# Kernel tuning notes

Measured on AMD Instinct MI355X. Metric: run time of the kernel, lower is better.

Reference implementation:

```python
import jax, jax.numpy as jnp
import numpy as np

N = 50000
IN_DIM = 512
OUT_DIM = 128
E = 800000
EPS = 1e-5


def setup_inputs() -> dict:
    key = jax.random.key(0)
    ks = jax.random.split(key, 12)
    x = jax.random.normal(ks[0], (N, IN_DIM), dtype=jnp.float32)
    edge_index = jax.random.randint(ks[1], (2, E), 0, N, dtype=jnp.int64)
    s1 = 1.0 / np.sqrt(IN_DIM)
    s2 = 1.0 / np.sqrt(OUT_DIM)
    W1 = jax.random.normal(ks[2], (IN_DIM, OUT_DIM), dtype=jnp.float32) * s1
    b1 = jnp.zeros((OUT_DIM,), jnp.float32)
    W2 = jax.random.normal(ks[3], (OUT_DIM, OUT_DIM), dtype=jnp.float32) * s2
    b2 = jnp.zeros((OUT_DIM,), jnp.float32)
    W3 = jax.random.normal(ks[4], (OUT_DIM, OUT_DIM), dtype=jnp.float32) * s2
    b3 = jnp.zeros((OUT_DIM,), jnp.float32)
    g1 = jnp.ones((OUT_DIM,), jnp.float32)
    be1 = jnp.zeros((OUT_DIM,), jnp.float32)
    g2 = jnp.ones((OUT_DIM,), jnp.float32)
    be2 = jnp.zeros((OUT_DIM,), jnp.float32)
    a1 = jnp.full((1,), 0.25, jnp.float32)  # PReLU weight
    a2 = jnp.full((1,), 0.25, jnp.float32)
    return {"x": x, "edge_index": edge_index, "W1": W1, "b1": b1, "W2": W2,
            "b2": b2, "W3": W3, "b3": b3, "g1": g1, "be1": be1, "g2": g2,
            "be2": be2, "a1": a1, "a2": a2}


def _gcn_norm(edge_index, n):
    # add self-loops, symmetric normalization deg^-1/2 A deg^-1/2
    loop = jnp.arange(n, dtype=edge_index.dtype)
    src = jnp.concatenate([edge_index[0], loop])
    dst = jnp.concatenate([edge_index[1], loop])
    deg = jax.ops.segment_sum(jnp.ones_like(dst, jnp.float32), dst, num_segments=n)
    dinv = jax.lax.rsqrt(jnp.maximum(deg, 1.0))
    norm = dinv[src] * dinv[dst]
    return src, dst, norm


def _gcn_conv(x, W, b, src, dst, norm, n):
    h = x @ W                                   # [N, out]
    msg = h[src] * norm[:, None]                # gather + scale over edges
    agg = jax.ops.segment_sum(msg, dst, num_segments=n)
    return agg + b


def _bn(x, g, b):
    mean = jnp.mean(x, axis=0)
    var = jnp.var(x, axis=0)  # biased, as torch BN uses for normalization
    return (x - mean) * jax.lax.rsqrt(var + EPS) * g + b


def _prelu(x, a):
    return jnp.where(x >= 0, x, a * x)


def reference(x, edge_index, W1, b1, W2, b2, W3, b3, g1, be1, g2, be2, a1, a2):
    src, dst, norm = _gcn_norm(edge_index, N)
    h = _gcn_conv(x, W1, b1, src, dst, norm, N)
    h = _prelu(_bn(h, g1, be1), a1)
    h = _gcn_conv(h, W2, b2, src, dst, norm, N)
    h = _prelu(_bn(h, g2, be2), a2)
    h = _gcn_conv(h, W3, b3, src, dst, norm, N)
    return h
```

## Files before the change

kernel.cpp:

```cpp
#include <hip/hip_runtime.h>

#define N_NODES 50000
#define IN_DIM  512
#define OUT_DIM 128
#define BN_EPS  1e-5f

typedef __attribute__((ext_vector_type(8))) short short8;
typedef __attribute__((ext_vector_type(4))) float f32x4;

__device__ __forceinline__ unsigned short bf16_rne(float x) {
    unsigned u = __float_as_uint(x);
    unsigned r = (u + 0x7FFFu + ((u >> 16) & 1u)) >> 16;
    return (unsigned short)r;
}
__device__ __forceinline__ float bf16_to_f(unsigned short s) {
    return __uint_as_float(((unsigned)s) << 16);
}

__device__ __forceinline__ void gload16(const void* g, void* l) {
    __builtin_amdgcn_global_load_lds(
        (const __attribute__((address_space(1))) void*)g,
        (__attribute__((address_space(3))) void*)l, 16, 0, 0);
}


__global__ void init_kernel(int* __restrict__ cnt, float* __restrict__ stats, int n) {
    int i = blockIdx.x * blockDim.x + threadIdx.x;
    if (i < n) cnt[i] = 1;
    if (i < 4096) stats[i] = 0.f;
}

__device__ __forceinline__ int edge_is64(const int* ei) {
    return (ei[1] | ei[3] | ei[5] | ei[7]) == 0;
}

__global__ void deg_kernel(const int* __restrict__ ei, int* __restrict__ cnt, int E) {
    int e = blockIdx.x * blockDim.x + threadIdx.x;
    if (e >= E) return;
    int dst;
    if (edge_is64(ei)) dst = ((const int2*)ei)[E + e].x;
    else               dst = ei[E + e];
    atomicAdd(&cnt[dst], 1);
}


__global__ __launch_bounds__(1024) void scan_partial(const int* __restrict__ cnt,
                                                     int* __restrict__ psum, int n) {
    __shared__ int wsum[16];
    const int i = blockIdx.x * 1024 + threadIdx.x;
    const int lane = threadIdx.x & 63;
    const int wv = threadIdx.x >> 6;
    int v = (i < n) ? cnt[i] : 0;
#pragma unroll
    for (int d = 1; d < 64; d <<= 1) v += __shfl_xor(v, d);
    if (lane == 0) wsum[wv] = v;
    __syncthreads();
    if (threadIdx.x == 0) {
        int t = 0;
#pragma unroll
        for (int w = 0; w < 16; ++w) t += wsum[w];
        psum[blockIdx.x] = t;
    }
}

__global__ void scan_base(const int* __restrict__ psum, int* __restrict__ pbase,
                          int* __restrict__ rowp, int nb, int n) {
    const int lane = threadIdx.x;
    int orig = (lane < nb) ? psum[lane] : 0;
    int v = orig;
#pragma unroll
    for (int d = 1; d < 64; d <<= 1) {
        int t = __shfl_up(v, d);
        if (lane >= d) v += t;
    }
    if (lane < nb) pbase[lane] = v - orig;
    if (lane == nb - 1) rowp[n] = v;
}

__global__ __launch_bounds__(1024) void scan_final(int* __restrict__ cnt,
                                                   const int* __restrict__ pbase,
                                                   int* __restrict__ rowp,
                                                   float* __restrict__ dinv,
                                                   unsigned short* __restrict__ col, int n) {
    __shared__ int wsum[16];
    const int i = blockIdx.x * 1024 + threadIdx.x;
    const int lane = threadIdx.x & 63;
    const int wv = threadIdx.x >> 6;
    int orig = (i < n) ? cnt[i] : 0;
    int v = orig;
#pragma unroll
    for (int d = 1; d < 64; d <<= 1) {
        int t = __shfl_up(v, d);
        if (lane >= d) v += t;
    }
    if (lane == 63) wsum[wv] = v;
    __syncthreads();
    int woff = 0;
    for (int w = 0; w < wv; ++w) woff += wsum[w];
    if (i < n) {
        int rp = pbase[blockIdx.x] + woff + v - orig;
        rowp[i] = rp;
        dinv[i] = rsqrtf(fmaxf((float)orig, 1.f));
        col[rp] = (unsigned short)i;
        cnt[i] = rp + 1;
    }
}

__global__ void fill_kernel(const int* __restrict__ ei, int* __restrict__ cnt,
                            unsigned short* __restrict__ col, int E) {
    int e = blockIdx.x * blockDim.x + threadIdx.x;
    if (e >= E) return;
    int src, dst;
    if (edge_is64(ei)) { src = ((const int2*)ei)[e].x; dst = ((const int2*)ei)[E + e].x; }
    else               { src = ei[e];                  dst = ei[E + e]; }
    int pos = atomicAdd(&cnt[dst], 1);
    col[pos] = (unsigned short)src;
}


__global__ __launch_bounds__(256) void wconv_all(const float* __restrict__ W1, short* __restrict__ Wt1,
                                                 const float* __restrict__ W2, short* __restrict__ Wt2,
                                                 const float* __restrict__ W3, short* __restrict__ Wt3) {
    __shared__ short tile[64][130];
    const int b = blockIdx.x;
    const float* W; short* Wt; int K, k0;
    if (b < 8)       { W = W1; Wt = Wt1; K = IN_DIM;  k0 = b * 64; }
    else if (b < 10) { W = W2; Wt = Wt2; K = OUT_DIM; k0 = (b - 8) * 64; }
    else             { W = W3; Wt = Wt3; K = OUT_DIM; k0 = (b - 10) * 64; }
    for (int i = threadIdx.x; i < 64 * 128; i += 256) {
        int k = i >> 7, c = i & 127;
        tile[k][c] = (short)bf16_rne(W[(size_t)(k0 + k) * 128 + c]);
    }
    __syncthreads();
    for (int i = threadIdx.x; i < 64 * 128; i += 256) {
        int c = i >> 6, k = i & 63;
        Wt[(size_t)c * K + k0 + k] = tile[k][c];
    }
}


template <typename TA, int K, bool XFORM>
__global__ __launch_bounds__(256) void mfma_gemm(
        const TA* __restrict__ A, const short* __restrict__ Wt,
        unsigned short* __restrict__ out, int M,
        const float* __restrict__ stats, const float* __restrict__ gam,
        const float* __restrict__ bet, const float* __restrict__ alpha_p,
        const float* __restrict__ dinv) {
    constexpr int BK = 64;
    constexpr int NSTEP = K / BK;
    constexpr int UPRA = (BK * (int)sizeof(TA)) / 16;
    constexpr int AINST = 64 * UPRA / 256;
    __shared__ TA    ldsA[64 * BK];
    __shared__ short ldsB[128 * BK];
    __shared__ float bnp[256];

    const int tid  = threadIdx.x;
    const int lane = tid & 63;
    const int wv   = tid >> 6;
    const int r16  = lane & 15;
    const int g    = lane >> 4;
    const int row0 = blockIdx.x * 64;
    const int arow_t = wv * 16 + r16;

    float alpha = 0.f;
    if constexpr (XFORM) {
        alpha = alpha_p[0];
        if (tid < 128) {
            float sum = 0.f, sq = 0.f;
#pragma unroll
            for (int r = 0; r < 8; ++r) {
                sum += stats[r * 256 + tid];
                sq  += stats[r * 256 + 128 + tid];
            }
            const float inv_n = 1.0f / (float)N_NODES;
            float mean = sum * inv_n;
            float var = fmaxf(sq * inv_n - mean * mean, 0.f);
            float sc = gam[tid] * rsqrtf(var + BN_EPS);
            bnp[tid] = sc;
            bnp[128 + tid] = bet[tid] - mean * sc;
        }
        __syncthreads();
    }

    f32x4 acc[8];
#pragma unroll
    for (int nf = 0; nf < 8; nf++) acc[nf] = (f32x4)(0.f);

    for (int s = 0; s < NSTEP; ++s) {
        const int k0 = s * BK;
        if (s) __syncthreads();
#pragma unroll
        for (int i = 0; i < AINST; ++i) {
            const int d   = i * 256 + tid;
            const int row = d / UPRA, p = d % UPRA;
            int grow = row0 + row; if (grow >= M) grow = M - 1;
            const char* src = (const char*)(A + (size_t)grow * K + k0) + ((p ^ (row & 7)) * 16);
            gload16(src, (char*)ldsA + (size_t)(i * 256 + wv * 64) * 16);
        }
#pragma unroll
        for (int i = 0; i < 4; ++i) {
            const int d    = i * 256 + tid;
            const int colb = d >> 3, p = d & 7;
            const short* src = Wt + (size_t)colb * K + k0 + (p ^ (colb & 7)) * 8;
            gload16(src, (char*)ldsB + (size_t)(i * 256 + wv * 64) * 16);
        }
        __syncthreads();
#pragma unroll
        for (int ksub = 0; ksub < 2; ++ksub) {
            short8 af;
            if constexpr (sizeof(TA) == 4) {
                const int q0 = ksub * 8 + g * 2;
                const float4* A4 = (const float4*)ldsA;
                float4 alo = A4[arow_t * UPRA + (q0 ^ (r16 & 7))];
                float4 ahi = A4[arow_t * UPRA + ((q0 + 1) ^ (r16 & 7))];
                float av[8] = {alo.x, alo.y, alo.z, alo.w, ahi.x, ahi.y, ahi.z, ahi.w};
#pragma unroll
                for (int j = 0; j < 8; j++) af[j] = (short)bf16_rne(av[j]);
            } else {
                short8 raw = ((const short8*)ldsA)[arow_t * 8 + ((ksub * 4 + g) ^ (r16 & 7))];
                if constexpr (XFORM) {
                    const int kk = ksub * 32 + g * 8;
                    const int kb = k0 + kk;
#pragma unroll
                    for (int j = 0; j < 8; j++) {
                        float v = fmaf(bf16_to_f((unsigned short)raw[j]), bnp[kb + j], bnp[128 + kb + j]);
                        v = v >= 0.f ? v : alpha * v;
                        af[j] = (short)bf16_rne(v);
                    }
                } else {
                    af = raw;
                }
            }
#pragma unroll
            for (int nf = 0; nf < 8; nf++) {
                const int colb = nf * 16 + r16;
                short8 bf = ((const short8*)ldsB)[colb * 8 + ((ksub * 4 + g) ^ (r16 & 7))];
                acc[nf] = __builtin_amdgcn_mfma_f32_16x16x32_bf16(af, bf, acc[nf], 0, 0, 0);
            }
        }
    }

    __syncthreads();
    unsigned short* ot = (unsigned short*)ldsB;
#pragma unroll
    for (int r = 0; r < 4; ++r) {
        const int trow = wv * 16 + g * 4 + r;
        const int grow = row0 + trow;
        const float dv = (grow < M) ? dinv[grow] : 0.f;
#pragma unroll
        for (int nf = 0; nf < 8; nf++)
            ot[trow * 128 + nf * 16 + r16] = bf16_rne(acc[nf][r] * dv);
    }
    __syncthreads();
    {
        const int trow = wv * 16 + r16;
        const int seg  = g;
        const int grow = row0 + trow;
        if (grow < M) {
            const float4* lsrc = (const float4*)ot + trow * 16 + seg * 4;
            float4* gdst = (float4*)((char*)out + (size_t)grow * 256) + seg * 4;
#pragma unroll
            for (int i = 0; i < 4; ++i) gdst[i] = lsrc[i];
        }
    }
}


template <int FINAL>
__global__ __launch_bounds__(256) void agg_kernel(
        const unsigned short* __restrict__ h, const int* __restrict__ rowp,
        const unsigned short* __restrict__ col, const float* __restrict__ dinv,
        const float* __restrict__ bias, void* __restrict__ outv,
        float* __restrict__ stats, int n) {
    const int wave = threadIdx.x >> 6;
    const int lane = threadIdx.x & 63;
    const int f = lane << 1;
    const float b0 = bias[f], b1 = bias[f + 1];
    float s0 = 0.f, s1 = 0.f, q0 = 0.f, q1 = 0.f;
    const int stride = gridDim.x << 2;
    for (int node = (blockIdx.x << 2) + wave; node < n; node += stride) {
        int e = rowp[node];
        const int end = rowp[node + 1];
        float a0 = 0.f, a1 = 0.f;
        for (; e + 8 <= end; e += 8) {
            int c[8];
#pragma unroll
            for (int j = 0; j < 8; j++) c[j] = col[e + j];
            unsigned v[8];
#pragma unroll
            for (int j = 0; j < 8; j++) v[j] = *(const unsigned*)(h + (size_t)c[j] * OUT_DIM + f);
#pragma unroll
            for (int j = 0; j < 8; j++) {
                a0 += __uint_as_float(v[j] << 16);
                a1 += __uint_as_float(v[j] & 0xFFFF0000u);
            }
        }
        for (; e < end; ++e) {
            unsigned v = *(const unsigned*)(h + (size_t)col[e] * OUT_DIM + f);
            a0 += __uint_as_float(v << 16);
            a1 += __uint_as_float(v & 0xFFFF0000u);
        }
        float dn = dinv[node];
        a0 = fmaf(a0, dn, b0);
        a1 = fmaf(a1, dn, b1);
        if (FINAL) {
            ((float2*)outv)[(size_t)node * 64 + lane] = make_float2(a0, a1);
        } else {
            unsigned p = ((unsigned)bf16_rne(a1) << 16) | (unsigned)bf16_rne(a0);
            ((unsigned*)outv)[(size_t)node * 64 + lane] = p;
            s0 += a0; s1 += a1;
            q0 = fmaf(a0, a0, q0); q1 = fmaf(a1, a1, q1);
        }
    }
    if (!FINAL) {
        __shared__ float red[4][256];
        red[wave][f] = s0;        red[wave][f + 1] = s1;
        red[wave][128 + f] = q0;  red[wave][128 + f + 1] = q1;
        __syncthreads();
        int t = threadIdx.x;
        float v = red[0][t] + red[1][t] + red[2][t] + red[3][t];
        atomicAdd(&stats[(blockIdx.x & 7) * 256 + t], v);
    }
}


extern "C" void kernel_launch(void* const* d_in, const int* in_sizes, int n_in,
                              void* d_out, int out_size, void* d_ws, size_t ws_size,
                              hipStream_t stream) {
    const float* x   = (const float*)d_in[0];
    const int*   ei  = (const int*)d_in[1];
    const float* W1  = (const float*)d_in[2];
    const float* b1  = (const float*)d_in[3];
    const float* W2  = (const float*)d_in[4];
    const float* b2  = (const float*)d_in[5];
    const float* W3  = (const float*)d_in[6];
    const float* b3  = (const float*)d_in[7];
    const float* g1  = (const float*)d_in[8];
    const float* be1 = (const float*)d_in[9];
    const float* g2  = (const float*)d_in[10];
    const float* be2 = (const float*)d_in[11];
    const float* a1  = (const float*)d_in[12];
    const float* a2  = (const float*)d_in[13];

    const int n = N_NODES;
    const int E = in_sizes[1] / 2;
    float* out = (float*)d_out;

    char* ws = (char*)d_ws;
    size_t off = 0;
    auto alloc = [&](size_t bytes) { void* p = ws + off; off += (bytes + 255) & ~(size_t)255; return p; };
    unsigned short* bufA = (unsigned short*)alloc((size_t)n * OUT_DIM * sizeof(short));
    unsigned short* hb   = (unsigned short*)alloc((size_t)n * OUT_DIM * sizeof(short));
    int*   cnt   = (int*)alloc((size_t)n * sizeof(int));
    int*   rowp  = (int*)alloc((size_t)(n + 1) * sizeof(int));
    float* dinv  = (float*)alloc((size_t)n * sizeof(float));
    unsigned short* col = (unsigned short*)alloc((size_t)(E + n) * sizeof(unsigned short));
    float* stats = (float*)alloc(4096 * sizeof(float));
    short* Wt1   = (short*)alloc((size_t)IN_DIM * OUT_DIM * sizeof(short));
    short* Wt2   = (short*)alloc((size_t)OUT_DIM * OUT_DIM * sizeof(short));
    short* Wt3   = (short*)alloc((size_t)OUT_DIM * OUT_DIM * sizeof(short));
    int*   psum  = (int*)alloc(64 * sizeof(int));
    int*   pbase = (int*)alloc(64 * sizeof(int));

    const int nbScan = (n + 1023) / 1024;

    hipLaunchKernelGGL(init_kernel, dim3((n + 255) / 256), dim3(256), 0, stream, cnt, stats, n);
    hipLaunchKernelGGL(deg_kernel, dim3((E + 255) / 256), dim3(256), 0, stream, ei, cnt, E);
    hipLaunchKernelGGL(scan_partial, dim3(nbScan), dim3(1024), 0, stream, cnt, psum, n);
    hipLaunchKernelGGL(scan_base, dim3(1), dim3(64), 0, stream, psum, pbase, rowp, nbScan, n);
    hipLaunchKernelGGL(scan_final, dim3(nbScan), dim3(1024), 0, stream, cnt, pbase, rowp, dinv, col, n);
    hipLaunchKernelGGL(fill_kernel, dim3((E + 255) / 256), dim3(256), 0, stream, ei, cnt, col, E);
    hipLaunchKernelGGL(wconv_all, dim3(12), dim3(256), 0, stream, W1, Wt1, W2, Wt2, W3, Wt3);

    const int gblocks = (n + 63) / 64;
    const int ablocks = 2048;
    hipLaunchKernelGGL((mfma_gemm<float, IN_DIM, false>), dim3(gblocks), dim3(256), 0, stream,
                       x, Wt1, bufA, n, nullptr, nullptr, nullptr, nullptr, dinv);
    hipLaunchKernelGGL((agg_kernel<0>), dim3(ablocks), dim3(256), 0, stream,
                       bufA, rowp, col, dinv, b1, hb, stats, n);
    hipLaunchKernelGGL((mfma_gemm<short, OUT_DIM, true>), dim3(gblocks), dim3(256), 0, stream,
                       (const short*)hb, Wt2, bufA, n, stats, g1, be1, a1, dinv);
    hipLaunchKernelGGL((agg_kernel<0>), dim3(ablocks), dim3(256), 0, stream,
                       bufA, rowp, col, dinv, b2, hb, stats + 2048, n);
    hipLaunchKernelGGL((mfma_gemm<short, OUT_DIM, true>), dim3(gblocks), dim3(256), 0, stream,
                       (const short*)hb, Wt3, bufA, n, stats + 2048, g2, be2, a2, dinv);
    hipLaunchKernelGGL((agg_kernel<1>), dim3(ablocks), dim3(256), 0, stream,
                       bufA, rowp, col, dinv, b3, out, nullptr, n);
}
```

Baseline: 280.9 us.

## Double-buffer GEMM LDS tiles and merge scan into single chained-lookback kernel

Replaces the three-kernel prefix scan (partial sums, base scan, final) with one kernel. Each block waits on its predecessor's inclusive sum through atomic acquire/release flags, which removes two launches. The GEMM now double-buffers its A and B LDS tiles so the next K-step's global-to-LDS loads are issued before the current step's MFMAs, overlapping memory with compute. The costs are twice the LDS (fp32 A for layer 1 becomes large), which may cut occupancy, and a serial spin chain in the scan that relies on blocks being scheduled in order.

```diff
diff --git a/kernel.cpp b/kernel.cpp
--- a/kernel.cpp
+++ b/kernel.cpp
@@ -1,4 +1,5 @@
 #include <hip/hip_runtime.h>
+#include <limits.h>
 
 #define N_NODES 50000
 #define IN_DIM  512
@@ -24,10 +25,12 @@
 }
 
 
-__global__ void init_kernel(int* __restrict__ cnt, float* __restrict__ stats, int n) {
+__global__ void init_kernel(int* __restrict__ cnt, float* __restrict__ stats,
+                            int* __restrict__ incl, int n) {
     int i = blockIdx.x * blockDim.x + threadIdx.x;
     if (i < n) cnt[i] = 1;
     if (i < 4096) stats[i] = 0.f;
+    if (i < 64) incl[i] = INT_MIN;
 }
 
 __device__ __forceinline__ int edge_is64(const int* ei) {
@@ -44,65 +47,47 @@
 }
 
 
-__global__ __launch_bounds__(1024) void scan_partial(const int* __restrict__ cnt,
-                                                     int* __restrict__ psum, int n) {
+__global__ __launch_bounds__(1024) void scan_lookback(int* __restrict__ cnt,
+                                                      int* __restrict__ incl,
+                                                      int* __restrict__ rowp,
+                                                      float* __restrict__ dinv,
+                                                      unsigned short* __restrict__ col, int n) {
     __shared__ int wsum[16];
-    const int i = blockIdx.x * 1024 + threadIdx.x;
-    const int lane = threadIdx.x & 63;
-    const int wv = threadIdx.x >> 6;
-    int v = (i < n) ? cnt[i] : 0;
-#pragma unroll
-    for (int d = 1; d < 64; d <<= 1) v += __shfl_xor(v, d);
-    if (lane == 0) wsum[wv] = v;
-    __syncthreads();
-    if (threadIdx.x == 0) {
-        int t = 0;
-#pragma unroll
-        for (int w = 0; w < 16; ++w) t += wsum[w];
-        psum[blockIdx.x] = t;
-    }
-}
-
-__global__ void scan_base(const int* __restrict__ psum, int* __restrict__ pbase,
-                          int* __restrict__ rowp, int nb, int n) {
-    const int lane = threadIdx.x;
-    int orig = (lane < nb) ? psum[lane] : 0;
+    __shared__ int sbase;
+    const int b = blockIdx.x;
+    const int tid = threadIdx.x;
+    const int i = b * 1024 + tid;
+    const int lane = tid & 63;
+    const int wv = tid >> 6;
+    int orig = (i < n) ? cnt[i] : 0;
     int v = orig;
 #pragma unroll
     for (int d = 1; d < 64; d <<= 1) {
         int t = __shfl_up(v, d);
         if (lane >= d) v += t;
     }
-    if (lane < nb) pbase[lane] = v - orig;
-    if (lane == nb - 1) rowp[n] = v;
-}
-
-__global__ __launch_bounds__(1024) void scan_final(int* __restrict__ cnt,
-                                                   const int* __restrict__ pbase,
-                                                   int* __restrict__ rowp,
-                                                   float* __restrict__ dinv,
-                                                   unsigned short* __restrict__ col, int n) {
-    __shared__ int wsum[16];
-    const int i = blockIdx.x * 1024 + threadIdx.x;
-    const int lane = threadIdx.x & 63;
-    const int wv = threadIdx.x >> 6;
-    int orig = (i < n) ? cnt[i] : 0;
-    int v = orig;
-#pragma unroll
-    for (int d = 1; d < 64; d <<= 1) {
-        int t = __shfl_up(v, d);
-        if (lane >= d) v += t;
-    }
     if (lane == 63) wsum[wv] = v;
     __syncthreads();
     int woff = 0;
     for (int w = 0; w < wv; ++w) woff += wsum[w];
+    if (tid == 1023) {
+        int base = 0;
+        if (b > 0) {
+            while ((base = __hip_atomic_load(&incl[b - 1], __ATOMIC_ACQUIRE,
+                                             __HIP_MEMORY_SCOPE_AGENT)) == INT_MIN) {}
+        }
+        __hip_atomic_store(&incl[b], base + woff + v, __ATOMIC_RELEASE,
+                           __HIP_MEMORY_SCOPE_AGENT);
+        sbase = base;
+    }
+    __syncthreads();
     if (i < n) {
-        int rp = pbase[blockIdx.x] + woff + v - orig;
+        int rp = sbase + woff + v - orig;
         rowp[i] = rp;
         dinv[i] = rsqrtf(fmaxf((float)orig, 1.f));
         col[rp] = (unsigned short)i;
         cnt[i] = rp + 1;
+        if (i == n - 1) rowp[n] = sbase + woff + v;
     }
 }
 
@@ -150,8 +135,8 @@
     constexpr int NSTEP = K / BK;
     constexpr int UPRA = (BK * (int)sizeof(TA)) / 16;
     constexpr int AINST = 64 * UPRA / 256;
-    __shared__ TA    ldsA[64 * BK];
-    __shared__ short ldsB[128 * BK];
+    __shared__ TA    ldsA[2][64 * BK];
+    __shared__ short ldsB[2][128 * BK];
     __shared__ float bnp[256];
 
     const int tid  = threadIdx.x;
@@ -161,6 +146,28 @@
     const int g    = lane >> 4;
     const int row0 = blockIdx.x * 64;
     const int arow_t = wv * 16 + r16;
+
+    auto stageA = [&](int bi, int k0) {
+#pragma unroll
+        for (int i = 0; i < AINST; ++i) {
+            const int d   = i * 256 + tid;
+            const int row = d / UPRA, p = d % UPRA;
+            int grow = row0 + row; if (grow >= M) grow = M - 1;
+            const char* src = (const char*)(A + (size_t)grow * K + k0) + ((p ^ (row & 7)) * 16);
+            gload16(src, (char*)ldsA[bi] + (size_t)(i * 256 + wv * 64) * 16);
+        }
+    };
+    auto stageB = [&](int bi, int k0) {
+#pragma unroll
+        for (int i = 0; i < 4; ++i) {
+            const int d    = i * 256 + tid;
+            const int colb = d >> 3, p = d & 7;
+            const short* src = Wt + (size_t)colb * K + k0 + (p ^ (colb & 7)) * 8;
+            gload16(src, (char*)ldsB[bi] + (size_t)(i * 256 + wv * 64) * 16);
+        }
+    };
+
+    stageA(0, 0); stageB(0, 0);
 
     float alpha = 0.f;
     if constexpr (XFORM) {
@@ -179,48 +186,36 @@
             bnp[tid] = sc;
             bnp[128 + tid] = bet[tid] - mean * sc;
         }
-        __syncthreads();
     }
 
     f32x4 acc[8];
 #pragma unroll
     for (int nf = 0; nf < 8; nf++) acc[nf] = (f32x4)(0.f);
 
+    __syncthreads();
+
     for (int s = 0; s < NSTEP; ++s) {
+        const int cur = s & 1;
+        if (s + 1 < NSTEP) {
+            stageA(cur ^ 1, (s + 1) * BK);
+            stageB(cur ^ 1, (s + 1) * BK);
+        }
         const int k0 = s * BK;
-        if (s) __syncthreads();
-#pragma unroll
-        for (int i = 0; i < AINST; ++i) {
-            const int d   = i * 256 + tid;
-            const int row = d / UPRA, p = d % UPRA;
-            int grow = row0 + row; if (grow >= M) grow = M - 1;
-            const char* src = (const char*)(A + (size_t)grow * K + k0) + ((p ^ (row & 7)) * 16);
-            gload16(src, (char*)ldsA + (size_t)(i * 256 + wv * 64) * 16);
-        }
-#pragma unroll
-        for (int i = 0; i < 4; ++i) {
-            const int d    = i * 256 + tid;
-            const int colb = d >> 3, p = d & 7;
-            const short* src = Wt + (size_t)colb * K + k0 + (p ^ (colb & 7)) * 8;
-            gload16(src, (char*)ldsB + (size_t)(i * 256 + wv * 64) * 16);
-        }
-        __syncthreads();
 #pragma unroll
         for (int ksub = 0; ksub < 2; ++ksub) {
             short8 af;
             if constexpr (sizeof(TA) == 4) {
                 const int q0 = ksub * 8 + g * 2;
-                const float4* A4 = (const float4*)ldsA;
+                const float4* A4 = (const float4*)ldsA[cur];
                 float4 alo = A4[arow_t * UPRA + (q0 ^ (r16 & 7))];
                 float4 ahi = A4[arow_t * UPRA + ((q0 + 1) ^ (r16 & 7))];
                 float av[8] = {alo.x, alo.y, alo.z, alo.w, ahi.x, ahi.y, ahi.z, ahi.w};
 #pragma unroll
                 for (int j = 0; j < 8; j++) af[j] = (short)bf16_rne(av[j]);
             } else {
-                short8 raw = ((const short8*)ldsA)[arow_t * 8 + ((ksub * 4 + g) ^ (r16 & 7))];
+                short8 raw = ((const short8*)ldsA[cur])[arow_t * 8 + ((ksub * 4 + g) ^ (r16 & 7))];
                 if constexpr (XFORM) {
-                    const int kk = ksub * 32 + g * 8;
-                    const int kb = k0 + kk;
+                    const int kb = k0 + ksub * 32 + g * 8;
 #pragma unroll
                     for (int j = 0; j < 8; j++) {
                         float v = fmaf(bf16_to_f((unsigned short)raw[j]), bnp[kb + j], bnp[128 + kb + j]);
@@ -234,13 +229,13 @@
 #pragma unroll
             for (int nf = 0; nf < 8; nf++) {
                 const int colb = nf * 16 + r16;
-                short8 bf = ((const short8*)ldsB)[colb * 8 + ((ksub * 4 + g) ^ (r16 & 7))];
+                short8 bf = ((const short8*)ldsB[cur])[colb * 8 + ((ksub * 4 + g) ^ (r16 & 7))];
                 acc[nf] = __builtin_amdgcn_mfma_f32_16x16x32_bf16(af, bf, acc[nf], 0, 0, 0);
             }
         }
-    }
-
-    __syncthreads();
+        __syncthreads();
+    }
+
     unsigned short* ot = (unsigned short*)ldsB;
 #pragma unroll
     for (int r = 0; r < 4; ++r) {
@@ -359,16 +354,13 @@
     short* Wt1   = (short*)alloc((size_t)IN_DIM * OUT_DIM * sizeof(short));
     short* Wt2   = (short*)alloc((size_t)OUT_DIM * OUT_DIM * sizeof(short));
     short* Wt3   = (short*)alloc((size_t)OUT_DIM * OUT_DIM * sizeof(short));
-    int*   psum  = (int*)alloc(64 * sizeof(int));
-    int*   pbase = (int*)alloc(64 * sizeof(int));
+    int*   incl  = (int*)alloc(64 * sizeof(int));
 
     const int nbScan = (n + 1023) / 1024;
 
-    hipLaunchKernelGGL(init_kernel, dim3((n + 255) / 256), dim3(256), 0, stream, cnt, stats, n);
+    hipLaunchKernelGGL(init_kernel, dim3((n + 255) / 256), dim3(256), 0, stream, cnt, stats, incl, n);
     hipLaunchKernelGGL(deg_kernel, dim3((E + 255) / 256), dim3(256), 0, stream, ei, cnt, E);
-    hipLaunchKernelGGL(scan_partial, dim3(nbScan), dim3(1024), 0, stream, cnt, psum, n);
-    hipLaunchKernelGGL(scan_base, dim3(1), dim3(64), 0, stream, psum, pbase, rowp, nbScan, n);
-    hipLaunchKernelGGL(scan_final, dim3(nbScan), dim3(1024), 0, stream, cnt, pbase, rowp, dinv, col, n);
+    hipLaunchKernelGGL(scan_lookback, dim3(nbScan), dim3(1024), 0, stream, cnt, incl, rowp, dinv, col, n);
     hipLaunchKernelGGL(fill_kernel, dim3((E + 255) / 256), dim3(256), 0, stream, ei, cnt, col, E);
     hipLaunchKernelGGL(wconv_all, dim3(12), dim3(256), 0, stream, W1, Wt1, W2, Wt2, W3, Wt3);
 
```

After: 332.2 us. 18.3% more time.
